# Optimization experiments

Measured on AMD Instinct MI355X. Metric: run time of the kernel, lower is better.

The kernel has to match this reference:

```python
import jax, jax.numpy as jnp
import numpy as np

E = 8        # num experts
TOP = 2      # top-k
D = 1024     # emb_size


def setup_inputs() -> dict:
    key = jax.random.key(0)
    ks = jax.random.split(key, 8)
    s = 1.0 / np.sqrt(D)
    x = jax.random.normal(ks[0], (4, 2048, D), dtype=jnp.float32)
    Wg = jax.random.uniform(ks[1], (D, E), jnp.float32, -s, s)
    bg = jax.random.uniform(ks[2], (E,), jnp.float32, -s, s)
    W1 = jax.random.uniform(ks[3], (E, D, D), jnp.float32, -s, s)
    b1 = jax.random.uniform(ks[4], (E, D), jnp.float32, -s, s)
    W2 = jax.random.uniform(ks[5], (E, D, D), jnp.float32, -s, s)
    b2 = jax.random.uniform(ks[6], (E, D), jnp.float32, -s, s)
    return {"x": x, "Wg": Wg, "bg": bg, "W1": W1, "b1": b1, "W2": W2, "b2": b2}


def reference(x, Wg, bg, W1, b1, W2, b2):
    x_shape = x.shape
    xt = x.reshape(-1, x_shape[-1])                       # [N, D] tokens
    gate_prob = jax.nn.softmax(xt @ Wg + bg, axis=-1)     # [N, E]
    top_w, top_i = jax.lax.top_k(gate_prob, TOP)          # [N, TOP]
    top_w = jax.nn.softmax(top_w, axis=-1)                # renormalize over top-k
    N = xt.shape[0]
    # combine weights scattered into dense [N, E] (each token has TOP nonzeros)
    comb = jnp.zeros((N, E), xt.dtype).at[jnp.arange(N)[:, None], top_i].add(top_w)
    # per-expert 2-layer MLP applied to all tokens; masked-out tokens get 0 combine weight
    h = jax.nn.relu(jnp.einsum('nd,edf->enf', xt, W1) + b1[:, None, :])   # [E, N, D]
    ye = jnp.einsum('enf,efg->eng', h, W2) + b2[:, None, :]               # [E, N, D]
    y = jnp.einsum('ne,eng->ng', comb, ye)                                # [N, D]
    return y.reshape(x_shape), gate_prob
```

## Files before the change

kernel.cpp:

```cpp
#include <hip/hip_runtime.h>
#include <stdint.h>

#define TOKENS 8192
#define DIM    1024
#define NEXP   8
#define NASSIGN (TOKENS*2)
#define BK     64

#define C_ROW   16
#define C_TILE  25
#define C_TOTAL 34

#define WS_CTRL  0
#define WS_TOPE  1024
#define WS_TOPW  (WS_TOPE + NASSIGN*4)
#define WS_PTOK  (WS_TOPW + NASSIGN*4)
#define WS_AROW  (WS_PTOK + NASSIGN*4)
#define WS_XB    (WS_AROW + NASSIGN*4)
#define WS_W1T   (WS_XB  + (size_t)TOKENS*DIM*2)
#define WS_W2T   (WS_W1T + (size_t)NEXP*DIM*DIM*2)
#define WS_H     (WS_W2T + (size_t)NEXP*DIM*DIM*2)
#define WS_YE    WS_XB

#define WGLD (DIM + 4)

typedef __attribute__((ext_vector_type(8))) short short8;
typedef __attribute__((ext_vector_type(4))) float floatx4;

__device__ __forceinline__ uint32_t bfr(float f) {
  uint32_t v = __float_as_uint(f);
  return (v + 0x7FFFu + ((v >> 16) & 1u)) >> 16;
}
__device__ __forceinline__ float b2f(uint32_t u) { return __uint_as_float(u << 16); }

__device__ __forceinline__ void load_lds16(const void* g, void* l) {
  __builtin_amdgcn_global_load_lds(
      (const __attribute__((address_space(1))) uint32_t*)g,
      (__attribute__((address_space(3))) uint32_t*)l, 16, 0, 0);
}

__global__ __launch_bounds__(256) void prep_kernel(
    const float* __restrict__ x, const float* __restrict__ Wg,
    const float* __restrict__ bg, float* __restrict__ gate_out,
    int* __restrict__ top_e, float* __restrict__ top_w,
    uint16_t* __restrict__ xb,
    const float* __restrict__ W1, const float* __restrict__ W2,
    uint16_t* __restrict__ W1T, uint16_t* __restrict__ W2T) {
  __shared__ __align__(16) char smem[NEXP * WGLD * 4];
  int t = threadIdx.x;

  if (blockIdx.x >= 2048) {
    uint16_t (*tile)[68] = (uint16_t (*)[68])smem;
    int cb = blockIdx.x - 2048;
    int m  = cb >> 8;
    int d0 = ((cb >> 4) & 15) * 64, f0 = (cb & 15) * 64;
    const float* src = (m < 8) ? (W1 + (size_t)m*DIM*DIM) : (W2 + (size_t)(m-8)*DIM*DIM);
    uint16_t*    dst = (m < 8) ? (W1T + (size_t)m*DIM*DIM) : (W2T + (size_t)(m-8)*DIM*DIM);
    int col = t & 63, rb = (t >> 6) * 16;
    #pragma unroll
    for (int i = 0; i < 16; i++) {
      int dr = rb + i;
      tile[dr][col] = (uint16_t)bfr(src[(size_t)(d0+dr)*DIM + f0 + col]);
    }
    __syncthreads();
    int dg = t & 15, frb = t >> 4;
    #pragma unroll
    for (int i = 0; i < 4; i++) {
      int fr = frb + i * 16;
      uint32_t b0 = tile[dg*4+0][fr], b1 = tile[dg*4+1][fr];
      uint32_t b2 = tile[dg*4+2][fr], b3 = tile[dg*4+3][fr];
      uint2 v;
      v.x = b0 | (b1 << 16);
      v.y = b2 | (b3 << 16);
      *(uint2*)&dst[(size_t)(f0+fr)*DIM + d0 + dg*4] = v;
    }
    return;
  }

  float* wgs = (float*)smem;
  #pragma unroll
  for (int k = 0; k < 32; k++) {
    int i = k * 256 + t;
    float v = Wg[i];
    wgs[(i & 7) * WGLD + (i >> 3)] = v;
  }
  __syncthreads();

  int wave = t >> 6, lane = t & 63;
  int tok = blockIdx.x * 4 + wave;
  const float4* xr = (const float4*)(x + (size_t)tok * DIM);
  uint2* xw = (uint2*)(xb + (size_t)tok * DIM);

  float4 acc[NEXP];
  #pragma unroll
  for (int e = 0; e < NEXP; e++) acc[e] = make_float4(0.f, 0.f, 0.f, 0.f);

  #pragma unroll
  for (int c = 0; c < 4; c++) {
    float4 xv = xr[c * 64 + lane];
    uint2 o;
    o.x = bfr(xv.x) | (bfr(xv.y) << 16);
    o.y = bfr(xv.z) | (bfr(xv.w) << 16);
    xw[c * 64 + lane] = o;
    int d0 = (c * 64 + lane) * 4;
    #pragma unroll
    for (int e = 0; e < NEXP; e++) {
      float4 wv = *(const float4*)&wgs[e * WGLD + d0];
      acc[e].x = fmaf(xv.x, wv.x, acc[e].x);
      acc[e].y = fmaf(xv.y, wv.y, acc[e].y);
      acc[e].z = fmaf(xv.z, wv.z, acc[e].z);
      acc[e].w = fmaf(xv.w, wv.w, acc[e].w);
    }
  }
  float s[NEXP];
  #pragma unroll
  for (int e = 0; e < NEXP; e++) s[e] = (acc[e].x + acc[e].y) + (acc[e].z + acc[e].w);
  #pragma unroll
  for (int off = 32; off > 0; off >>= 1) {
    #pragma unroll
    for (int e = 0; e < NEXP; e++) s[e] += __shfl_xor(s[e], off);
  }
  if (lane == 0) {
    float lg[NEXP], p[NEXP];
    float mx = -1e30f;
    #pragma unroll
    for (int e = 0; e < NEXP; e++) { lg[e] = s[e] + bg[e]; mx = fmaxf(mx, lg[e]); }
    float sum = 0.f;
    #pragma unroll
    for (int e = 0; e < NEXP; e++) { p[e] = expf(lg[e] - mx); sum += p[e]; }
    float inv = 1.f / sum;
    #pragma unroll
    for (int e = 0; e < NEXP; e++) p[e] *= inv;
    float4* go = (float4*)(gate_out + (size_t)tok * NEXP);
    go[0] = make_float4(p[0], p[1], p[2], p[3]);
    go[1] = make_float4(p[4], p[5], p[6], p[7]);
    int i1 = 0;
    #pragma unroll
    for (int e = 1; e < NEXP; e++) if (p[e] > p[i1]) i1 = e;
    int i2 = (i1 == 0) ? 1 : 0;
    #pragma unroll
    for (int e = 0; e < NEXP; e++) if (e != i1 && p[e] > p[i2]) i2 = e;
    float ev = expf(p[i2] - p[i1]);
    float w1 = 1.f / (1.f + ev), w2 = ev / (1.f + ev);
    top_e[2*tok]   = i1; top_e[2*tok+1] = i2;
    top_w[2*tok]   = w1; top_w[2*tok+1] = w2;
  }
}

__global__ __launch_bounds__(1024) void route_kernel(
    const int* __restrict__ top_e, int* __restrict__ ctrl,
    int* __restrict__ ptok, int* __restrict__ arow) {
  __shared__ int sc[NEXP * 1024];
  __shared__ int scnt[NEXP];
  __shared__ int rowstart[NEXP];
  int t = threadIdx.x;
  int e_loc[16];
  int cnt[NEXP];
  #pragma unroll
  for (int e = 0; e < NEXP; e++) cnt[e] = 0;
  #pragma unroll
  for (int j = 0; j < 16; j++) {
    int e = top_e[t * 16 + j];
    e_loc[j] = e;
    cnt[e]++;
  }
  #pragma unroll
  for (int e = 0; e < NEXP; e++) sc[e * 1024 + t] = cnt[e];
  __syncthreads();
  int wave = t >> 6, lane = t & 63;
  if (wave < NEXP) {
    int running = 0;
    for (int chunk = 0; chunk < 16; chunk++) {
      int idx = wave * 1024 + chunk * 64 + lane;
      int v = sc[idx];
      int incl = v;
      #pragma unroll
      for (int off = 1; off < 64; off <<= 1) {
        int u = __shfl_up(incl, off);
        if (lane >= off) incl += u;
      }
      sc[idx] = running + incl - v;
      running += __shfl(incl, 63);
    }
    if (lane == 0) scnt[wave] = running;
  }
  __syncthreads();
  if (t == 0) {
    int rs = 0, ts = 0;
    for (int e = 0; e < NEXP; e++) {
      ctrl[C_ROW + e] = rs;
      ctrl[C_TILE + e] = ts;
      rowstart[e] = rs;
      int c = scnt[e];
      rs += c;
      ts += (c + 127) >> 7;
    }
    ctrl[C_ROW + NEXP] = rs;
    ctrl[C_TILE + NEXP] = ts;
    ctrl[C_TOTAL] = ts;
  }
  __syncthreads();
  int off[NEXP];
  #pragma unroll
  for (int e = 0; e < NEXP; e++) off[e] = rowstart[e] + sc[e * 1024 + t];
  #pragma unroll
  for (int j = 0; j < 16; j++) {
    int i = t * 16 + j;
    int e = e_loc[j];
    int pos = off[e]++;
    ptok[pos] = i >> 1;
    arow[i] = pos;
  }
}

__device__ __forceinline__ bool sched_map(const int* ctrl, int bid,
                                          int& mtile, int& n0) {
  int total = ctrl[C_TOTAL];
  int spx = (total + 7) >> 3;
  int xcd = bid & 7, j = bid >> 3;
  int slot = j >> 3;
  if (slot >= spx) return false;
  mtile = xcd * spx + slot;
  n0 = (j & 7) * 128;
  return mtile < total;
}

__global__ __launch_bounds__(256, 2) void gemm1_kernel(
    const uint16_t* __restrict__ xb, const uint16_t* __restrict__ w1t,
    const float* __restrict__ b1, const int* __restrict__ ctrl,
    const int* __restrict__ ptok, uint16_t* __restrict__ h) {
  __shared__ __align__(16) uint16_t As[128*BK];
  __shared__ __align__(16) uint16_t Bs[128*BK];
  int mtile, n0;
  if (!sched_map(ctrl, blockIdx.x, mtile, n0)) return;
  int e = 0;
  #pragma unroll
  for (int k = 1; k < NEXP; k++) if (mtile >= ctrl[C_TILE + k]) e = k;
  int row0 = ctrl[C_ROW + e] + (mtile - ctrl[C_TILE + e]) * 128;
  int rend = ctrl[C_ROW + e + 1];

  int t = threadIdx.x, lane = t & 63, w = t >> 6;
  const uint16_t* gA[4];
  const uint16_t* gB[4];
  #pragma unroll
  for (int i = 0; i < 4; i++) {
    int s = i * 256 + t;
    int row = s >> 3, cs = s & 7;
    int gc = cs ^ (row & 7);
    int ar = row0 + row; if (ar > NASSIGN-1) ar = NASSIGN-1;
    int tok = ptok[ar];
    gA[i] = xb  + (size_t)tok * DIM + gc*8;
    gB[i] = w1t + (size_t)e*DIM*DIM + (size_t)(n0 + row)*DIM + gc*8;
  }
  floatx4 acc[4][4];
  #pragma unroll
  for (int mi = 0; mi < 4; mi++)
    #pragma unroll
    for (int ni = 0; ni < 4; ni++) acc[mi][ni] = (floatx4)(0.f);

  int wm = w & 1, wn = w >> 1;
  int l15 = lane & 15, lq = lane >> 4;

  for (int kt = 0; kt < DIM/BK; kt++) {
    #pragma unroll
    for (int i = 0; i < 4; i++) {
      load_lds16(gA[i], &As[(i*256 + t) * 8]);
      load_lds16(gB[i], &Bs[(i*256 + t) * 8]);
      gA[i] += BK; gB[i] += BK;
    }
    __syncthreads();
    #pragma unroll
    for (int ks = 0; ks < 2; ks++) {
      short8 a[4], b[4];
      #pragma unroll
      for (int mi = 0; mi < 4; mi++) {
        int row = wm*64 + mi*16 + l15;
        int slot = (ks*4 + lq) ^ (row & 7);
        a[mi] = *(const short8*)&As[row*BK + slot*8];
      }
      #pragma unroll
      for (int ni = 0; ni < 4; ni++) {
        int row = wn*64 + ni*16 + l15;
        int slot = (ks*4 + lq) ^ (row & 7);
        b[ni] = *(const short8*)&Bs[row*BK + slot*8];
      }
      #pragma unroll
      for (int mi = 0; mi < 4; mi++)
        #pragma unroll
        for (int ni = 0; ni < 4; ni++)
          acc[mi][ni] = __builtin_amdgcn_mfma_f32_16x16x32_bf16(a[mi], b[ni], acc[mi][ni], 0, 0, 0);
    }
    __syncthreads();
  }
  #pragma unroll
  for (int mi = 0; mi < 4; mi++) {
    #pragma unroll
    for (int r = 0; r < 4; r++) {
      int rt = wm*64 + mi*16 + lq*4 + r;
      int ar = row0 + rt;
      if (ar < rend) {
        #pragma unroll
        for (int ni = 0; ni < 4; ni++) {
          int n = n0 + wn*64 + ni*16 + l15;
          float v = acc[mi][ni][r] + b1[e*DIM + n];
          v = fmaxf(v, 0.f);
          h[(size_t)ar*DIM + n] = (uint16_t)bfr(v);
        }
      }
    }
  }
}

__global__ __launch_bounds__(256, 2) void gemm2_kernel(
    const uint16_t* __restrict__ h, const uint16_t* __restrict__ w2t,
    const float* __restrict__ b2, const int* __restrict__ ctrl,
    uint16_t* __restrict__ yeb) {
  __shared__ __align__(16) uint16_t As[128*BK];
  __shared__ __align__(16) uint16_t Bs[128*BK];
  int mtile, n0;
  if (!sched_map(ctrl, blockIdx.x, mtile, n0)) return;
  int e = 0;
  #pragma unroll
  for (int k = 1; k < NEXP; k++) if (mtile >= ctrl[C_TILE + k]) e = k;
  int row0 = ctrl[C_ROW + e] + (mtile - ctrl[C_TILE + e]) * 128;
  int rend = ctrl[C_ROW + e + 1];

  int t = threadIdx.x, lane = t & 63, w = t >> 6;
  const uint16_t* gA[4];
  const uint16_t* gB[4];
  #pragma unroll
  for (int i = 0; i < 4; i++) {
    int s = i * 256 + t;
    int row = s >> 3, cs = s & 7;
    int gc = cs ^ (row & 7);
    int ar = row0 + row; if (ar > NASSIGN-1) ar = NASSIGN-1;
    gA[i] = h   + (size_t)ar * DIM + gc*8;
    gB[i] = w2t + (size_t)e*DIM*DIM + (size_t)(n0 + row)*DIM + gc*8;
  }
  floatx4 acc[4][4];
  #pragma unroll
  for (int mi = 0; mi < 4; mi++)
    #pragma unroll
    for (int ni = 0; ni < 4; ni++) acc[mi][ni] = (floatx4)(0.f);

  int wm = w & 1, wn = w >> 1;
  int l15 = lane & 15, lq = lane >> 4;

  for (int kt = 0; kt < DIM/BK; kt++) {
    #pragma unroll
    for (int i = 0; i < 4; i++) {
      load_lds16(gA[i], &As[(i*256 + t) * 8]);
      load_lds16(gB[i], &Bs[(i*256 + t) * 8]);
      gA[i] += BK; gB[i] += BK;
    }
    __syncthreads();
    #pragma unroll
    for (int ks = 0; ks < 2; ks++) {
      short8 a[4], b[4];
      #pragma unroll
      for (int mi = 0; mi < 4; mi++) {
        int row = wm*64 + mi*16 + l15;
        int slot = (ks*4 + lq) ^ (row & 7);
        a[mi] = *(const short8*)&As[row*BK + slot*8];
      }
      #pragma unroll
      for (int ni = 0; ni < 4; ni++) {
        int row = wn*64 + ni*16 + l15;
        int slot = (ks*4 + lq) ^ (row & 7);
        b[ni] = *(const short8*)&Bs[row*BK + slot*8];
      }
      #pragma unroll
      for (int mi = 0; mi < 4; mi++)
        #pragma unroll
        for (int ni = 0; ni < 4; ni++)
          acc[mi][ni] = __builtin_amdgcn_mfma_f32_16x16x32_bf16(a[mi], b[ni], acc[mi][ni], 0, 0, 0);
    }
    __syncthreads();
  }
  #pragma unroll
  for (int mi = 0; mi < 4; mi++) {
    #pragma unroll
    for (int r = 0; r < 4; r++) {
      int rt = wm*64 + mi*16 + lq*4 + r;
      int ar = row0 + rt;
      if (ar < rend) {
        #pragma unroll
        for (int ni = 0; ni < 4; ni++) {
          int n = n0 + wn*64 + ni*16 + l15;
          float v = acc[mi][ni][r] + b2[e*DIM + n];
          yeb[(size_t)ar*DIM + n] = (uint16_t)bfr(v);
        }
      }
    }
  }
}

__global__ __launch_bounds__(256) void combine_kernel(
    const uint16_t* __restrict__ yeb, const int* __restrict__ arow,
    const float* __restrict__ top_w, float* __restrict__ y) {
  int tok = blockIdx.x, t = threadIdx.x;
  int r0 = arow[2*tok], r1 = arow[2*tok+1];
  float w0 = top_w[2*tok], w1 = top_w[2*tok+1];
  const uint2* a = (const uint2*)(yeb + (size_t)r0 * DIM);
  const uint2* b = (const uint2*)(yeb + (size_t)r1 * DIM);
  uint2 av = a[t], bv = b[t];
  float4 o;
  o.x = w0 * b2f(av.x & 0xFFFFu) + w1 * b2f(bv.x & 0xFFFFu);
  o.y = w0 * b2f(av.x >> 16)     + w1 * b2f(bv.x >> 16);
  o.z = w0 * b2f(av.y & 0xFFFFu) + w1 * b2f(bv.y & 0xFFFFu);
  o.w = w0 * b2f(av.y >> 16)     + w1 * b2f(bv.y >> 16);
  ((float4*)(y + (size_t)tok * DIM))[t] = o;
}

extern "C" void kernel_launch(void* const* d_in, const int* in_sizes, int n_in,
                              void* d_out, int out_size, void* d_ws, size_t ws_size,
                              hipStream_t stream) {
  const float* x  = (const float*)d_in[0];
  const float* Wg = (const float*)d_in[1];
  const float* bg = (const float*)d_in[2];
  const float* W1 = (const float*)d_in[3];
  const float* b1 = (const float*)d_in[4];
  const float* W2 = (const float*)d_in[5];
  const float* b2 = (const float*)d_in[6];
  float* out = (float*)d_out;
  char* ws = (char*)d_ws;

  int*      ctrl = (int*)(ws + WS_CTRL);
  int*      tope = (int*)(ws + WS_TOPE);
  float*    topw = (float*)(ws + WS_TOPW);
  int*      ptok = (int*)(ws + WS_PTOK);
  int*      arow = (int*)(ws + WS_AROW);
  uint16_t* xb   = (uint16_t*)(ws + WS_XB);
  uint16_t* w1t  = (uint16_t*)(ws + WS_W1T);
  uint16_t* w2t  = (uint16_t*)(ws + WS_W2T);
  uint16_t* hbuf = (uint16_t*)(ws + WS_H);
  uint16_t* yeb  = (uint16_t*)(ws + WS_YE);

  prep_kernel<<<6144, 256, 0, stream>>>(x, Wg, bg, out + (size_t)TOKENS*DIM,
                                        tope, topw, xb, W1, W2, w1t, w2t);
  route_kernel<<<1, 1024, 0, stream>>>(tope, ctrl, ptok, arow);

  gemm1_kernel<<<136*8, 256, 0, stream>>>(xb, w1t, b1, ctrl, ptok, hbuf);
  gemm2_kernel<<<136*8, 256, 0, stream>>>(hbuf, w2t, b2, ctrl, yeb);
  combine_kernel<<<TOKENS, 256, 0, stream>>>(yeb, arow, topw, out);
}
```

Measured before the change: 267.9 us.

## Fuse combine into gemm2 epilogue via weighted atomicAdd into zeroed output

```diff
diff --git a/kernel.cpp b/kernel.cpp
--- a/kernel.cpp
+++ b/kernel.cpp
@@ -15,12 +15,11 @@
 #define WS_TOPE  1024
 #define WS_TOPW  (WS_TOPE + NASSIGN*4)
 #define WS_PTOK  (WS_TOPW + NASSIGN*4)
-#define WS_AROW  (WS_PTOK + NASSIGN*4)
-#define WS_XB    (WS_AROW + NASSIGN*4)
+#define WS_PW    (WS_PTOK + NASSIGN*4)
+#define WS_XB    (WS_PW   + NASSIGN*4)
 #define WS_W1T   (WS_XB  + (size_t)TOKENS*DIM*2)
 #define WS_W2T   (WS_W1T + (size_t)NEXP*DIM*DIM*2)
 #define WS_H     (WS_W2T + (size_t)NEXP*DIM*DIM*2)
-#define WS_YE    WS_XB
 
 #define WGLD (DIM + 4)
 
@@ -31,7 +30,6 @@
   uint32_t v = __float_as_uint(f);
   return (v + 0x7FFFu + ((v >> 16) & 1u)) >> 16;
 }
-__device__ __forceinline__ float b2f(uint32_t u) { return __uint_as_float(u << 16); }
 
 __device__ __forceinline__ void load_lds16(const void* g, void* l) {
   __builtin_amdgcn_global_load_lds(
@@ -148,8 +146,8 @@
 }
 
 __global__ __launch_bounds__(1024) void route_kernel(
-    const int* __restrict__ top_e, int* __restrict__ ctrl,
-    int* __restrict__ ptok, int* __restrict__ arow) {
+    const int* __restrict__ top_e, const float* __restrict__ top_w,
+    int* __restrict__ ctrl, int* __restrict__ ptok, float* __restrict__ pw) {
   __shared__ int sc[NEXP * 1024];
   __shared__ int scnt[NEXP];
   __shared__ int rowstart[NEXP];
@@ -209,7 +207,7 @@
     int e = e_loc[j];
     int pos = off[e]++;
     ptok[pos] = i >> 1;
-    arow[i] = pos;
+    pw[pos] = top_w[i];
   }
 }
 
@@ -225,7 +223,7 @@
   return mtile < total;
 }
 
-__global__ __launch_bounds__(256, 2) void gemm1_kernel(
+__global__ __launch_bounds__(256, 4) void gemm1_kernel(
     const uint16_t* __restrict__ xb, const uint16_t* __restrict__ w1t,
     const float* __restrict__ b1, const int* __restrict__ ctrl,
     const int* __restrict__ ptok, uint16_t* __restrict__ h) {
@@ -311,10 +309,11 @@
   }
 }
 
-__global__ __launch_bounds__(256, 2) void gemm2_kernel(
+__global__ __launch_bounds__(256, 4) void gemm2_kernel(
     const uint16_t* __restrict__ h, const uint16_t* __restrict__ w2t,
     const float* __restrict__ b2, const int* __restrict__ ctrl,
-    uint16_t* __restrict__ yeb) {
+    const int* __restrict__ ptok, const float* __restrict__ pw,
+    float* __restrict__ y) {
   __shared__ __align__(16) uint16_t As[128*BK];
   __shared__ __align__(16) uint16_t Bs[128*BK];
   int mtile, n0;
@@ -384,32 +383,17 @@
       int rt = wm*64 + mi*16 + lq*4 + r;
       int ar = row0 + rt;
       if (ar < rend) {
+        int tok = ptok[ar];
+        float wv = pw[ar];
         #pragma unroll
         for (int ni = 0; ni < 4; ni++) {
           int n = n0 + wn*64 + ni*16 + l15;
-          float v = acc[mi][ni][r] + b2[e*DIM + n];
-          yeb[(size_t)ar*DIM + n] = (uint16_t)bfr(v);
+          float v = (acc[mi][ni][r] + b2[e*DIM + n]) * wv;
+          atomicAdd(&y[(size_t)tok*DIM + n], v);
         }
       }
     }
   }
-}
-
-__global__ __launch_bounds__(256) void combine_kernel(
-    const uint16_t* __restrict__ yeb, const int* __restrict__ arow,
-    const float* __restrict__ top_w, float* __restrict__ y) {
-  int tok = blockIdx.x, t = threadIdx.x;
-  int r0 = arow[2*tok], r1 = arow[2*tok+1];
-  float w0 = top_w[2*tok], w1 = top_w[2*tok+1];
-  const uint2* a = (const uint2*)(yeb + (size_t)r0 * DIM);
-  const uint2* b = (const uint2*)(yeb + (size_t)r1 * DIM);
-  uint2 av = a[t], bv = b[t];
-  float4 o;
-  o.x = w0 * b2f(av.x & 0xFFFFu) + w1 * b2f(bv.x & 0xFFFFu);
-  o.y = w0 * b2f(av.x >> 16)     + w1 * b2f(bv.x >> 16);
-  o.z = w0 * b2f(av.y & 0xFFFFu) + w1 * b2f(bv.y & 0xFFFFu);
-  o.w = w0 * b2f(av.y >> 16)     + w1 * b2f(bv.y >> 16);
-  ((float4*)(y + (size_t)tok * DIM))[t] = o;
 }
 
 extern "C" void kernel_launch(void* const* d_in, const int* in_sizes, int n_in,
@@ -429,18 +413,18 @@
   int*      tope = (int*)(ws + WS_TOPE);
   float*    topw = (float*)(ws + WS_TOPW);
   int*      ptok = (int*)(ws + WS_PTOK);
-  int*      arow = (int*)(ws + WS_AROW);
+  float*    pwv  = (float*)(ws + WS_PW);
   uint16_t* xb   = (uint16_t*)(ws + WS_XB);
   uint16_t* w1t  = (uint16_t*)(ws + WS_W1T);
   uint16_t* w2t  = (uint16_t*)(ws + WS_W2T);
   uint16_t* hbuf = (uint16_t*)(ws + WS_H);
-  uint16_t* yeb  = (uint16_t*)(ws + WS_YE);
+
+  hipMemsetAsync(out, 0, (size_t)TOKENS*DIM*sizeof(float), stream);
 
   prep_kernel<<<6144, 256, 0, stream>>>(x, Wg, bg, out + (size_t)TOKENS*DIM,
                                         tope, topw, xb, W1, W2, w1t, w2t);
-  route_kernel<<<1, 1024, 0, stream>>>(tope, ctrl, ptok, arow);
+  route_kernel<<<1, 1024, 0, stream>>>(tope, topw, ctrl, ptok, pwv);
 
   gemm1_kernel<<<136*8, 256, 0, stream>>>(xb, w1t, b1, ctrl, ptok, hbuf);
-  gemm2_kernel<<<136*8, 256, 0, stream>>>(hbuf, w2t, b2, ctrl, yeb);
-  combine_kernel<<<TOKENS, 256, 0, stream>>>(yeb, arow, topw, out);
-}
+  gemm2_kernel<<<136*8, 256, 0, stream>>>(hbuf, w2t, b2, ctrl, ptok, pwv, out);
+}
```

New measurement: 388.8 us. 1.45x slower.
